# Kernel tuning notes

Measured on AMD Instinct MI355X. Metric: run time of the kernel, lower is better.

## Reference

```python
import jax, jax.numpy as jnp
import numpy as np

T = 8388608  # sequence length (2^23)
WIDTH = 1.0


def phi(x, width=WIDTH):
    # Phi(x) = x if x > 0; x + width if x < -width; 0 otherwise
    return jnp.maximum(x, 0.0) + jnp.minimum(x + width, 0.0)


def setup_inputs() -> dict:
    key = jax.random.key(0)
    k1, k2 = jax.random.split(key)
    inputs = jax.random.normal(k1, (1, T), dtype=jnp.float32)
    state = jnp.zeros((1, 1), dtype=jnp.float32)
    # non_neg constrained scalar weight
    kernel = jax.random.uniform(k2, (1, 1), dtype=jnp.float32)
    return {"inputs": inputs, "state": state, "kernel": kernel}


def reference(inputs, state, kernel):
    # outputs_ = inputs * kernel (scalar multiply), then sequential hysteresis scan:
    #   out_i = Phi(outputs_[i] - out_{i-1}) + out_{i-1}
    xs = (inputs * kernel[0, 0])[0]  # [T]

    def step(prev, x):
        out = phi(x - prev) + prev
        return out, out

    last, outs = jax.lax.scan(step, state[0, 0], xs)
    outputs = outs.reshape(inputs.shape)       # [1, T]
    new_state = last.reshape(1, 1)             # [1, 1]
    return outputs, new_state
```

## Files before the change

### kernel.cpp

```cpp
#include <hip/hip_runtime.h>
#include <math.h>


#define TPB 256
#define SEGS 8
#define WAVES (TPB / 64)
#define ELEMS (TPB * SEGS * 4)

__device__ __forceinline__ float clampf(float x, float lo, float hi) {
    return fminf(fmaxf(x, lo), hi);
}

__global__ __launch_bounds__(TPB) void k_agg(const float4* __restrict__ x4,
                                             const float* __restrict__ kern,
                                             float2* __restrict__ agg) {
    __shared__ float wtlo[SEGS][WAVES], wthi[SEGS][WAVES];
    const int t = threadIdx.x, lane = t & 63, w = t >> 6;
    const int b = blockIdx.x;
    const float k = kern[0];
    const size_t base4 = (size_t)b * (TPB * SEGS);

#pragma unroll
    for (int s = 0; s < SEGS; ++s) {
        float4 v = x4[base4 + (size_t)s * TPB + t];
        float a0 = v.x * k, a1 = v.y * k, a2 = v.z * k, a3 = v.w * k;
        float lo = a0, hi = a0 + 1.0f;
        lo = clampf(lo, a1, a1 + 1.0f); hi = clampf(hi, a1, a1 + 1.0f);
        lo = clampf(lo, a2, a2 + 1.0f); hi = clampf(hi, a2, a2 + 1.0f);
        lo = clampf(lo, a3, a3 + 1.0f); hi = clampf(hi, a3, a3 + 1.0f);
#pragma unroll
        for (int off = 1; off < 64; off <<= 1) {
            float plo = __shfl_down(lo, off);
            float phi_ = __shfl_down(hi, off);
            float nlo = clampf(lo, plo, phi_);
            float nhi = clampf(hi, plo, phi_);
            lo = nlo; hi = nhi;
        }
        if (lane == 0) { wtlo[s][w] = lo; wthi[s][w] = hi; }
    }
    __syncthreads();
    if (t == 0) {
        float Alo = -INFINITY, Ahi = INFINITY;
#pragma unroll
        for (int s = 0; s < SEGS; ++s)
#pragma unroll
            for (int i = 0; i < WAVES; ++i) {
                Alo = clampf(Alo, wtlo[s][i], wthi[s][i]);
                Ahi = clampf(Ahi, wtlo[s][i], wthi[s][i]);
            }
        agg[b] = make_float2(Alo, Ahi);
    }
}

__global__ __launch_bounds__(TPB) void k_apply(
    const float4* __restrict__ x4,
    const float* __restrict__ kern,
    const float* __restrict__ state,
    const float2* __restrict__ agg,
    float* __restrict__ out,
    int nblocks)
{
    __shared__ float wtlo[SEGS][WAVES], wthi[SEGS][WAVES];
    __shared__ float rlo[WAVES], rhi[WAVES];
    __shared__ float s_vb;

    const int t = threadIdx.x, lane = t & 63, w = t >> 6;
    const int b = blockIdx.x;
    const float k = kern[0];
    const size_t base4 = (size_t)b * (TPB * SEGS);

    float eslo[SEGS], eshi[SEGS];
    float Slo[SEGS], Shi[SEGS];

#pragma unroll
    for (int s = 0; s < SEGS; ++s) {
        float4 v = x4[base4 + (size_t)s * TPB + t];
        float a0 = v.x * k, a1 = v.y * k, a2 = v.z * k, a3 = v.w * k;
        float lo = a0, hi = a0 + 1.0f;
        lo = clampf(lo, a1, a1 + 1.0f); hi = clampf(hi, a1, a1 + 1.0f);
        lo = clampf(lo, a2, a2 + 1.0f); hi = clampf(hi, a2, a2 + 1.0f);
        lo = clampf(lo, a3, a3 + 1.0f); hi = clampf(hi, a3, a3 + 1.0f);
#pragma unroll
        for (int off = 1; off < 64; off <<= 1) {
            float plo = __shfl_up(lo, off);
            float phi_ = __shfl_up(hi, off);
            if (lane >= off) {
                float nlo = clampf(plo, lo, hi);
                float nhi = clampf(phi_, lo, hi);
                lo = nlo; hi = nhi;
            }
        }
        float elo = __shfl_up(lo, 1), ehi = __shfl_up(hi, 1);
        if (lane == 0) { elo = -INFINITY; ehi = INFINITY; }
        eslo[s] = elo; eshi[s] = ehi;
        if (lane == 63) { wtlo[s][w] = lo; wthi[s][w] = hi; }
    }
    __syncthreads();

#pragma unroll
    for (int s = 0; s < SEGS; ++s) {
        float welo = -INFINITY, wehi = INFINITY;
        for (int i = 0; i < w; ++i) {
            welo = clampf(welo, wtlo[s][i], wthi[s][i]);
            wehi = clampf(wehi, wtlo[s][i], wthi[s][i]);
        }
        float llo = eslo[s], lhi = eshi[s];
        eslo[s] = clampf(welo, llo, lhi);
        eshi[s] = clampf(wehi, llo, lhi);
        float stl = -INFINITY, sth = INFINITY;
#pragma unroll
        for (int i = 0; i < WAVES; ++i) {
            stl = clampf(stl, wtlo[s][i], wthi[s][i]);
            sth = clampf(sth, wtlo[s][i], wthi[s][i]);
        }
        Slo[s] = stl; Shi[s] = sth;
    }

    {
        const int per = nblocks / TPB;
        float lo = -INFINITY, hi = INFINITY;
        for (int c = 0; c < per; ++c) {
            int j = t * per + c;
            if (j < b) {
                float2 ag = agg[j];
                lo = clampf(lo, ag.x, ag.y);
                hi = clampf(hi, ag.x, ag.y);
            }
        }
#pragma unroll
        for (int off = 1; off < 64; off <<= 1) {
            float plo = __shfl_down(lo, off);
            float phi_ = __shfl_down(hi, off);
            float nlo = clampf(lo, plo, phi_);
            float nhi = clampf(hi, plo, phi_);
            lo = nlo; hi = nhi;
        }
        if (lane == 0) { rlo[w] = lo; rhi[w] = hi; }
        __syncthreads();
        if (t == 0) {
            float Plo = rlo[0], Phi = rhi[0];
#pragma unroll
            for (int i = 1; i < WAVES; ++i) {
                Plo = clampf(Plo, rlo[i], rhi[i]);
                Phi = clampf(Phi, rlo[i], rhi[i]);
            }
            s_vb = clampf(state[0], Plo, Phi);
        }
        __syncthreads();
    }

    float p = s_vb;
    float4* out4 = (float4*)out;
#pragma unroll
    for (int s = 0; s < SEGS; ++s) {
        float wv = clampf(p, eslo[s], eshi[s]);
        float4 v = x4[base4 + (size_t)s * TPB + t];
        float a0 = v.x * k, a1 = v.y * k, a2 = v.z * k, a3 = v.w * k;
        float4 r;
        wv = clampf(wv, a0, a0 + 1.0f); r.x = wv;
        wv = clampf(wv, a1, a1 + 1.0f); r.y = wv;
        wv = clampf(wv, a2, a2 + 1.0f); r.z = wv;
        wv = clampf(wv, a3, a3 + 1.0f); r.w = wv;
        out4[base4 + (size_t)s * TPB + t] = r;
        p = clampf(p, Slo[s], Shi[s]);
    }

    if (b == nblocks - 1 && t == 0) {
        float q = s_vb;
#pragma unroll
        for (int s = 0; s < SEGS; ++s) q = clampf(q, Slo[s], Shi[s]);
        out[(size_t)nblocks * ELEMS] = q;
    }
}

extern "C" void kernel_launch(void* const* d_in, const int* in_sizes, int n_in,
                              void* d_out, int out_size, void* d_ws, size_t ws_size,
                              hipStream_t stream) {
    const float4* x4   = (const float4*)d_in[0];
    const float* state = (const float*)d_in[1];
    const float* kern  = (const float*)d_in[2];
    float* out = (float*)d_out;

    const size_t T = (size_t)in_sizes[0];
    const int nblocks = (int)(T / ELEMS);
    float2* agg = (float2*)d_ws;

    k_agg<<<nblocks, TPB, 0, stream>>>(x4, kern, agg);
    k_apply<<<nblocks, TPB, 0, stream>>>(x4, kern, state, agg, out, nblocks);
}
```

Before: 101.7 us.

## Switch to contiguous per-thread chunks with register-held inputs in scan kernels

Each thread now owns 32 contiguous elements instead of strided float4 segments. The per-thread composition runs serially in registers, so only one wave scan per block is needed instead of eight. The apply kernel keeps the scaled inputs in a register array and reuses them, which avoids reading the input from global memory twice. The cost is higher register pressure (32 floats per thread) and non-coalesced strided float4 accesses, since adjacent threads read addresses 128 bytes apart.

```diff
diff --git a/kernel.cpp b/kernel.cpp
--- a/kernel.cpp
+++ b/kernel.cpp
@@ -3,9 +3,9 @@
 
 
 #define TPB 256
-#define SEGS 8
 #define WAVES (TPB / 64)
-#define ELEMS (TPB * SEGS * 4)
+#define PT 32
+#define ELEMS (TPB * PT)
 
 __device__ __forceinline__ float clampf(float x, float lo, float hi) {
     return fminf(fmaxf(x, lo), hi);
@@ -14,41 +14,40 @@
 __global__ __launch_bounds__(TPB) void k_agg(const float4* __restrict__ x4,
                                              const float* __restrict__ kern,
                                              float2* __restrict__ agg) {
-    __shared__ float wtlo[SEGS][WAVES], wthi[SEGS][WAVES];
+    __shared__ float wl[WAVES], wh[WAVES];
     const int t = threadIdx.x, lane = t & 63, w = t >> 6;
     const int b = blockIdx.x;
     const float k = kern[0];
-    const size_t base4 = (size_t)b * (TPB * SEGS);
 
+    const float4* p = x4 + (size_t)b * (ELEMS / 4) + (size_t)t * (PT / 4);
+    float lo = -INFINITY, hi = INFINITY;
 #pragma unroll
-    for (int s = 0; s < SEGS; ++s) {
-        float4 v = x4[base4 + (size_t)s * TPB + t];
-        float a0 = v.x * k, a1 = v.y * k, a2 = v.z * k, a3 = v.w * k;
-        float lo = a0, hi = a0 + 1.0f;
-        lo = clampf(lo, a1, a1 + 1.0f); hi = clampf(hi, a1, a1 + 1.0f);
-        lo = clampf(lo, a2, a2 + 1.0f); hi = clampf(hi, a2, a2 + 1.0f);
-        lo = clampf(lo, a3, a3 + 1.0f); hi = clampf(hi, a3, a3 + 1.0f);
+    for (int i = 0; i < PT / 4; ++i) {
+        float4 v = p[i];
+        float a;
+        a = v.x * k; lo = clampf(lo, a, a + 1.0f); hi = clampf(hi, a, a + 1.0f);
+        a = v.y * k; lo = clampf(lo, a, a + 1.0f); hi = clampf(hi, a, a + 1.0f);
+        a = v.z * k; lo = clampf(lo, a, a + 1.0f); hi = clampf(hi, a, a + 1.0f);
+        a = v.w * k; lo = clampf(lo, a, a + 1.0f); hi = clampf(hi, a, a + 1.0f);
+    }
 #pragma unroll
-        for (int off = 1; off < 64; off <<= 1) {
-            float plo = __shfl_down(lo, off);
-            float phi_ = __shfl_down(hi, off);
-            float nlo = clampf(lo, plo, phi_);
-            float nhi = clampf(hi, plo, phi_);
-            lo = nlo; hi = nhi;
-        }
-        if (lane == 0) { wtlo[s][w] = lo; wthi[s][w] = hi; }
+    for (int off = 1; off < 64; off <<= 1) {
+        float plo = __shfl_down(lo, off);
+        float phi_ = __shfl_down(hi, off);
+        float nlo = clampf(lo, plo, phi_);
+        float nhi = clampf(hi, plo, phi_);
+        lo = nlo; hi = nhi;
     }
+    if (lane == 0) { wl[w] = lo; wh[w] = hi; }
     __syncthreads();
     if (t == 0) {
-        float Alo = -INFINITY, Ahi = INFINITY;
+        float L = wl[0], H = wh[0];
 #pragma unroll
-        for (int s = 0; s < SEGS; ++s)
-#pragma unroll
-            for (int i = 0; i < WAVES; ++i) {
-                Alo = clampf(Alo, wtlo[s][i], wthi[s][i]);
-                Ahi = clampf(Ahi, wtlo[s][i], wthi[s][i]);
-            }
-        agg[b] = make_float2(Alo, Ahi);
+        for (int i = 1; i < WAVES; ++i) {
+            L = clampf(L, wl[i], wh[i]);
+            H = clampf(H, wl[i], wh[i]);
+        }
+        agg[b] = make_float2(L, H);
     }
 }
 
@@ -60,65 +59,18 @@
     float* __restrict__ out,
     int nblocks)
 {
-    __shared__ float wtlo[SEGS][WAVES], wthi[SEGS][WAVES];
-    __shared__ float rlo[WAVES], rhi[WAVES];
+    __shared__ float rl[WAVES], rh[WAVES];
+    __shared__ float wtl[WAVES], wth[WAVES];
     __shared__ float s_vb;
 
     const int t = threadIdx.x, lane = t & 63, w = t >> 6;
     const int b = blockIdx.x;
     const float k = kern[0];
-    const size_t base4 = (size_t)b * (TPB * SEGS);
-
-    float eslo[SEGS], eshi[SEGS];
-    float Slo[SEGS], Shi[SEGS];
-
-#pragma unroll
-    for (int s = 0; s < SEGS; ++s) {
-        float4 v = x4[base4 + (size_t)s * TPB + t];
-        float a0 = v.x * k, a1 = v.y * k, a2 = v.z * k, a3 = v.w * k;
-        float lo = a0, hi = a0 + 1.0f;
-        lo = clampf(lo, a1, a1 + 1.0f); hi = clampf(hi, a1, a1 + 1.0f);
-        lo = clampf(lo, a2, a2 + 1.0f); hi = clampf(hi, a2, a2 + 1.0f);
-        lo = clampf(lo, a3, a3 + 1.0f); hi = clampf(hi, a3, a3 + 1.0f);
-#pragma unroll
-        for (int off = 1; off < 64; off <<= 1) {
-            float plo = __shfl_up(lo, off);
-            float phi_ = __shfl_up(hi, off);
-            if (lane >= off) {
-                float nlo = clampf(plo, lo, hi);
-                float nhi = clampf(phi_, lo, hi);
-                lo = nlo; hi = nhi;
-            }
-        }
-        float elo = __shfl_up(lo, 1), ehi = __shfl_up(hi, 1);
-        if (lane == 0) { elo = -INFINITY; ehi = INFINITY; }
-        eslo[s] = elo; eshi[s] = ehi;
-        if (lane == 63) { wtlo[s][w] = lo; wthi[s][w] = hi; }
-    }
-    __syncthreads();
-
-#pragma unroll
-    for (int s = 0; s < SEGS; ++s) {
-        float welo = -INFINITY, wehi = INFINITY;
-        for (int i = 0; i < w; ++i) {
-            welo = clampf(welo, wtlo[s][i], wthi[s][i]);
-            wehi = clampf(wehi, wtlo[s][i], wthi[s][i]);
-        }
-        float llo = eslo[s], lhi = eshi[s];
-        eslo[s] = clampf(welo, llo, lhi);
-        eshi[s] = clampf(wehi, llo, lhi);
-        float stl = -INFINITY, sth = INFINITY;
-#pragma unroll
-        for (int i = 0; i < WAVES; ++i) {
-            stl = clampf(stl, wtlo[s][i], wthi[s][i]);
-            sth = clampf(sth, wtlo[s][i], wthi[s][i]);
-        }
-        Slo[s] = stl; Shi[s] = sth;
-    }
 
     {
         const int per = nblocks / TPB;
         float lo = -INFINITY, hi = INFINITY;
+#pragma unroll
         for (int c = 0; c < per; ++c) {
             int j = t * per + c;
             if (j < b) {
@@ -135,42 +87,67 @@
             float nhi = clampf(hi, plo, phi_);
             lo = nlo; hi = nhi;
         }
-        if (lane == 0) { rlo[w] = lo; rhi[w] = hi; }
-        __syncthreads();
-        if (t == 0) {
-            float Plo = rlo[0], Phi = rhi[0];
+        if (lane == 0) { rl[w] = lo; rh[w] = hi; }
+    }
+    __syncthreads();
+    if (t == 0) {
+        float L = rl[0], H = rh[0];
 #pragma unroll
-            for (int i = 1; i < WAVES; ++i) {
-                Plo = clampf(Plo, rlo[i], rhi[i]);
-                Phi = clampf(Phi, rlo[i], rhi[i]);
-            }
-            s_vb = clampf(state[0], Plo, Phi);
+        for (int i = 1; i < WAVES; ++i) {
+            L = clampf(L, rl[i], rh[i]);
+            H = clampf(H, rl[i], rh[i]);
         }
-        __syncthreads();
+        s_vb = clampf(state[0], L, H);
     }
 
-    float p = s_vb;
-    float4* out4 = (float4*)out;
+    const float4* p = x4 + (size_t)b * (ELEMS / 4) + (size_t)t * (PT / 4);
+    float a[PT];
+    float lo = -INFINITY, hi = INFINITY;
 #pragma unroll
-    for (int s = 0; s < SEGS; ++s) {
-        float wv = clampf(p, eslo[s], eshi[s]);
-        float4 v = x4[base4 + (size_t)s * TPB + t];
-        float a0 = v.x * k, a1 = v.y * k, a2 = v.z * k, a3 = v.w * k;
-        float4 r;
-        wv = clampf(wv, a0, a0 + 1.0f); r.x = wv;
-        wv = clampf(wv, a1, a1 + 1.0f); r.y = wv;
-        wv = clampf(wv, a2, a2 + 1.0f); r.z = wv;
-        wv = clampf(wv, a3, a3 + 1.0f); r.w = wv;
-        out4[base4 + (size_t)s * TPB + t] = r;
-        p = clampf(p, Slo[s], Shi[s]);
+    for (int i = 0; i < PT / 4; ++i) {
+        float4 v = p[i];
+        a[4 * i + 0] = v.x * k; a[4 * i + 1] = v.y * k;
+        a[4 * i + 2] = v.z * k; a[4 * i + 3] = v.w * k;
+#pragma unroll
+        for (int c = 0; c < 4; ++c) {
+            float q = a[4 * i + c];
+            lo = clampf(lo, q, q + 1.0f);
+            hi = clampf(hi, q, q + 1.0f);
+        }
     }
 
-    if (b == nblocks - 1 && t == 0) {
-        float q = s_vb;
 #pragma unroll
-        for (int s = 0; s < SEGS; ++s) q = clampf(q, Slo[s], Shi[s]);
-        out[(size_t)nblocks * ELEMS] = q;
+    for (int off = 1; off < 64; off <<= 1) {
+        float plo = __shfl_up(lo, off);
+        float phi_ = __shfl_up(hi, off);
+        if (lane >= off) {
+            float nlo = clampf(plo, lo, hi);
+            float nhi = clampf(phi_, lo, hi);
+            lo = nlo; hi = nhi;
+        }
     }
+    float elo = __shfl_up(lo, 1), ehi = __shfl_up(hi, 1);
+    if (lane == 0) { elo = -INFINITY; ehi = INFINITY; }
+    if (lane == 63) { wtl[w] = lo; wth[w] = hi; }
+    __syncthreads();
+
+    float v = s_vb;
+    for (int i = 0; i < w; ++i) v = clampf(v, wtl[i], wth[i]);
+    v = clampf(v, elo, ehi);
+
+    float4* o = (float4*)(out + (size_t)b * ELEMS + (size_t)t * PT);
+#pragma unroll
+    for (int i = 0; i < PT / 4; ++i) {
+        float4 r;
+        v = clampf(v, a[4 * i + 0], a[4 * i + 0] + 1.0f); r.x = v;
+        v = clampf(v, a[4 * i + 1], a[4 * i + 1] + 1.0f); r.y = v;
+        v = clampf(v, a[4 * i + 2], a[4 * i + 2] + 1.0f); r.z = v;
+        v = clampf(v, a[4 * i + 3], a[4 * i + 3] + 1.0f); r.w = v;
+        o[i] = r;
+    }
+
+    if (b == nblocks - 1 && t == TPB - 1)
+        out[(size_t)nblocks * ELEMS] = v;
 }
 
 extern "C" void kernel_launch(void* const* d_in, const int* in_sizes, int n_in,
```

New measurement: 100.6 us. No clear change (-1.0%).

## Keep scaled inputs in registers, eight floats per lane, hoist cross-block prefix

Applied to the files above, without the earlier changes.

Each lane now processes eight contiguous floats per segment using two float4 loads, with four segments instead of eight, so per-lane serial composition is longer and the shuffle-scan count halves. k_apply keeps the scaled inputs in registers instead of reloading them from global memory in the final write pass, and it computes the cross-block prefix from the aggregates before the local scan so that latency can overlap. The final state is now taken from the last thread's output value. This uses more registers per thread and trades some coalescing granularity for fewer shuffle rounds.

```diff
diff --git a/kernel.cpp b/kernel.cpp
--- a/kernel.cpp
+++ b/kernel.cpp
@@ -3,9 +3,11 @@
 
 
 #define TPB 256
-#define SEGS 8
 #define WAVES (TPB / 64)
-#define ELEMS (TPB * SEGS * 4)
+#define SEGS 4
+#define FPL 8
+#define SEG_ELEMS (TPB * FPL)
+#define ELEMS (SEGS * SEG_ELEMS)
 
 __device__ __forceinline__ float clampf(float x, float lo, float hi) {
     return fminf(fmaxf(x, lo), hi);
@@ -14,20 +16,25 @@
 __global__ __launch_bounds__(TPB) void k_agg(const float4* __restrict__ x4,
                                              const float* __restrict__ kern,
                                              float2* __restrict__ agg) {
-    __shared__ float wtlo[SEGS][WAVES], wthi[SEGS][WAVES];
+    __shared__ float wl[SEGS][WAVES], wh[SEGS][WAVES];
     const int t = threadIdx.x, lane = t & 63, w = t >> 6;
     const int b = blockIdx.x;
     const float k = kern[0];
-    const size_t base4 = (size_t)b * (TPB * SEGS);
-
-#pragma unroll
-    for (int s = 0; s < SEGS; ++s) {
-        float4 v = x4[base4 + (size_t)s * TPB + t];
-        float a0 = v.x * k, a1 = v.y * k, a2 = v.z * k, a3 = v.w * k;
-        float lo = a0, hi = a0 + 1.0f;
-        lo = clampf(lo, a1, a1 + 1.0f); hi = clampf(hi, a1, a1 + 1.0f);
-        lo = clampf(lo, a2, a2 + 1.0f); hi = clampf(hi, a2, a2 + 1.0f);
-        lo = clampf(lo, a3, a3 + 1.0f); hi = clampf(hi, a3, a3 + 1.0f);
+    const size_t base4 = (size_t)b * (ELEMS / 4);
+
+#pragma unroll
+    for (int s = 0; s < SEGS; ++s) {
+        const size_t i4 = base4 + (size_t)s * (SEG_ELEMS / 4) + (size_t)t * 2;
+        float4 v0 = x4[i4], v1 = x4[i4 + 1];
+        float lo, hi, a;
+        a = v0.x * k; lo = a; hi = a + 1.0f;
+        a = v0.y * k; lo = clampf(lo, a, a + 1.0f); hi = clampf(hi, a, a + 1.0f);
+        a = v0.z * k; lo = clampf(lo, a, a + 1.0f); hi = clampf(hi, a, a + 1.0f);
+        a = v0.w * k; lo = clampf(lo, a, a + 1.0f); hi = clampf(hi, a, a + 1.0f);
+        a = v1.x * k; lo = clampf(lo, a, a + 1.0f); hi = clampf(hi, a, a + 1.0f);
+        a = v1.y * k; lo = clampf(lo, a, a + 1.0f); hi = clampf(hi, a, a + 1.0f);
+        a = v1.z * k; lo = clampf(lo, a, a + 1.0f); hi = clampf(hi, a, a + 1.0f);
+        a = v1.w * k; lo = clampf(lo, a, a + 1.0f); hi = clampf(hi, a, a + 1.0f);
 #pragma unroll
         for (int off = 1; off < 64; off <<= 1) {
             float plo = __shfl_down(lo, off);
@@ -36,19 +43,19 @@
             float nhi = clampf(hi, plo, phi_);
             lo = nlo; hi = nhi;
         }
-        if (lane == 0) { wtlo[s][w] = lo; wthi[s][w] = hi; }
+        if (lane == 0) { wl[s][w] = lo; wh[s][w] = hi; }
     }
     __syncthreads();
     if (t == 0) {
-        float Alo = -INFINITY, Ahi = INFINITY;
+        float L = -INFINITY, H = INFINITY;
 #pragma unroll
         for (int s = 0; s < SEGS; ++s)
 #pragma unroll
             for (int i = 0; i < WAVES; ++i) {
-                Alo = clampf(Alo, wtlo[s][i], wthi[s][i]);
-                Ahi = clampf(Ahi, wtlo[s][i], wthi[s][i]);
+                L = clampf(L, wl[s][i], wh[s][i]);
+                H = clampf(H, wl[s][i], wh[s][i]);
             }
-        agg[b] = make_float2(Alo, Ahi);
+        agg[b] = make_float2(L, H);
     }
 }
 
@@ -60,26 +67,64 @@
     float* __restrict__ out,
     int nblocks)
 {
-    __shared__ float wtlo[SEGS][WAVES], wthi[SEGS][WAVES];
-    __shared__ float rlo[WAVES], rhi[WAVES];
+    __shared__ float rl[WAVES], rh[WAVES];
+    __shared__ float wtl[SEGS][WAVES], wth[SEGS][WAVES];
     __shared__ float s_vb;
 
     const int t = threadIdx.x, lane = t & 63, w = t >> 6;
     const int b = blockIdx.x;
     const float k = kern[0];
-    const size_t base4 = (size_t)b * (TPB * SEGS);
-
+    const size_t base4 = (size_t)b * (ELEMS / 4);
+
+    {
+        const int per = nblocks / TPB;
+        float lo = -INFINITY, hi = INFINITY;
+#pragma unroll
+        for (int c = 0; c < per; ++c) {
+            int j = t * per + c;
+            if (j < b) {
+                float2 ag = agg[j];
+                lo = clampf(lo, ag.x, ag.y);
+                hi = clampf(hi, ag.x, ag.y);
+            }
+        }
+#pragma unroll
+        for (int off = 1; off < 64; off <<= 1) {
+            float plo = __shfl_down(lo, off);
+            float phi_ = __shfl_down(hi, off);
+            float nlo = clampf(lo, plo, phi_);
+            float nhi = clampf(hi, plo, phi_);
+            lo = nlo; hi = nhi;
+        }
+        if (lane == 0) { rl[w] = lo; rh[w] = hi; }
+    }
+    __syncthreads();
+    if (t == 0) {
+        float L = rl[0], H = rh[0];
+#pragma unroll
+        for (int i = 1; i < WAVES; ++i) {
+            L = clampf(L, rl[i], rh[i]);
+            H = clampf(H, rl[i], rh[i]);
+        }
+        s_vb = clampf(state[0], L, H);
+    }
+
+    float a[SEGS][FPL];
     float eslo[SEGS], eshi[SEGS];
     float Slo[SEGS], Shi[SEGS];
 
 #pragma unroll
     for (int s = 0; s < SEGS; ++s) {
-        float4 v = x4[base4 + (size_t)s * TPB + t];
-        float a0 = v.x * k, a1 = v.y * k, a2 = v.z * k, a3 = v.w * k;
-        float lo = a0, hi = a0 + 1.0f;
-        lo = clampf(lo, a1, a1 + 1.0f); hi = clampf(hi, a1, a1 + 1.0f);
-        lo = clampf(lo, a2, a2 + 1.0f); hi = clampf(hi, a2, a2 + 1.0f);
-        lo = clampf(lo, a3, a3 + 1.0f); hi = clampf(hi, a3, a3 + 1.0f);
+        const size_t i4 = base4 + (size_t)s * (SEG_ELEMS / 4) + (size_t)t * 2;
+        float4 v0 = x4[i4], v1 = x4[i4 + 1];
+        a[s][0] = v0.x * k; a[s][1] = v0.y * k; a[s][2] = v0.z * k; a[s][3] = v0.w * k;
+        a[s][4] = v1.x * k; a[s][5] = v1.y * k; a[s][6] = v1.z * k; a[s][7] = v1.w * k;
+        float lo = a[s][0], hi = a[s][0] + 1.0f;
+#pragma unroll
+        for (int c = 1; c < FPL; ++c) {
+            lo = clampf(lo, a[s][c], a[s][c] + 1.0f);
+            hi = clampf(hi, a[s][c], a[s][c] + 1.0f);
+        }
 #pragma unroll
         for (int off = 1; off < 64; off <<= 1) {
             float plo = __shfl_up(lo, off);
@@ -93,7 +138,7 @@
         float elo = __shfl_up(lo, 1), ehi = __shfl_up(hi, 1);
         if (lane == 0) { elo = -INFINITY; ehi = INFINITY; }
         eslo[s] = elo; eshi[s] = ehi;
-        if (lane == 63) { wtlo[s][w] = lo; wthi[s][w] = hi; }
+        if (lane == 63) { wtl[s][w] = lo; wth[s][w] = hi; }
     }
     __syncthreads();
 
@@ -101,8 +146,8 @@
     for (int s = 0; s < SEGS; ++s) {
         float welo = -INFINITY, wehi = INFINITY;
         for (int i = 0; i < w; ++i) {
-            welo = clampf(welo, wtlo[s][i], wthi[s][i]);
-            wehi = clampf(wehi, wtlo[s][i], wthi[s][i]);
+            welo = clampf(welo, wtl[s][i], wth[s][i]);
+            wehi = clampf(wehi, wtl[s][i], wth[s][i]);
         }
         float llo = eslo[s], lhi = eshi[s];
         eslo[s] = clampf(welo, llo, lhi);
@@ -110,67 +155,34 @@
         float stl = -INFINITY, sth = INFINITY;
 #pragma unroll
         for (int i = 0; i < WAVES; ++i) {
-            stl = clampf(stl, wtlo[s][i], wthi[s][i]);
-            sth = clampf(sth, wtlo[s][i], wthi[s][i]);
+            stl = clampf(stl, wtl[s][i], wth[s][i]);
+            sth = clampf(sth, wtl[s][i], wth[s][i]);
         }
         Slo[s] = stl; Shi[s] = sth;
     }
 
-    {
-        const int per = nblocks / TPB;
-        float lo = -INFINITY, hi = INFINITY;
-        for (int c = 0; c < per; ++c) {
-            int j = t * per + c;
-            if (j < b) {
-                float2 ag = agg[j];
-                lo = clampf(lo, ag.x, ag.y);
-                hi = clampf(hi, ag.x, ag.y);
-            }
-        }
-#pragma unroll
-        for (int off = 1; off < 64; off <<= 1) {
-            float plo = __shfl_down(lo, off);
-            float phi_ = __shfl_down(hi, off);
-            float nlo = clampf(lo, plo, phi_);
-            float nhi = clampf(hi, plo, phi_);
-            lo = nlo; hi = nhi;
-        }
-        if (lane == 0) { rlo[w] = lo; rhi[w] = hi; }
-        __syncthreads();
-        if (t == 0) {
-            float Plo = rlo[0], Phi = rhi[0];
-#pragma unroll
-            for (int i = 1; i < WAVES; ++i) {
-                Plo = clampf(Plo, rlo[i], rhi[i]);
-                Phi = clampf(Phi, rlo[i], rhi[i]);
-            }
-            s_vb = clampf(state[0], Plo, Phi);
-        }
-        __syncthreads();
-    }
-
+    __syncthreads();
     float p = s_vb;
-    float4* out4 = (float4*)out;
-#pragma unroll
-    for (int s = 0; s < SEGS; ++s) {
-        float wv = clampf(p, eslo[s], eshi[s]);
-        float4 v = x4[base4 + (size_t)s * TPB + t];
-        float a0 = v.x * k, a1 = v.y * k, a2 = v.z * k, a3 = v.w * k;
-        float4 r;
-        wv = clampf(wv, a0, a0 + 1.0f); r.x = wv;
-        wv = clampf(wv, a1, a1 + 1.0f); r.y = wv;
-        wv = clampf(wv, a2, a2 + 1.0f); r.z = wv;
-        wv = clampf(wv, a3, a3 + 1.0f); r.w = wv;
-        out4[base4 + (size_t)s * TPB + t] = r;
+    float wv = p;
+#pragma unroll
+    for (int s = 0; s < SEGS; ++s) {
+        wv = clampf(p, eslo[s], eshi[s]);
+        float4 r0, r1;
+        wv = clampf(wv, a[s][0], a[s][0] + 1.0f); r0.x = wv;
+        wv = clampf(wv, a[s][1], a[s][1] + 1.0f); r0.y = wv;
+        wv = clampf(wv, a[s][2], a[s][2] + 1.0f); r0.z = wv;
+        wv = clampf(wv, a[s][3], a[s][3] + 1.0f); r0.w = wv;
+        wv = clampf(wv, a[s][4], a[s][4] + 1.0f); r1.x = wv;
+        wv = clampf(wv, a[s][5], a[s][5] + 1.0f); r1.y = wv;
+        wv = clampf(wv, a[s][6], a[s][6] + 1.0f); r1.z = wv;
+        wv = clampf(wv, a[s][7], a[s][7] + 1.0f); r1.w = wv;
+        float4* o = (float4*)(out + (size_t)b * ELEMS + (size_t)s * SEG_ELEMS) + (size_t)t * 2;
+        o[0] = r0; o[1] = r1;
         p = clampf(p, Slo[s], Shi[s]);
     }
 
-    if (b == nblocks - 1 && t == 0) {
-        float q = s_vb;
-#pragma unroll
-        for (int s = 0; s < SEGS; ++s) q = clampf(q, Slo[s], Shi[s]);
-        out[(size_t)nblocks * ELEMS] = q;
-    }
+    if (b == nblocks - 1 && t == TPB - 1)
+        out[(size_t)nblocks * ELEMS] = wv;
 }
 
 extern "C" void kernel_launch(void* const* d_in, const int* in_sizes, int n_in,
```

Result: faster. 97.97 us (-3.6%).
